# Optimization experiments

Hardware: AMD Instinct MI355X
Metric: run time of the kernel (lower is better)

## Reference

```python
import jax, jax.numpy as jnp
import numpy as np

NC = 80          # classes
REG_MAX = 16     # DFL bins
NK = 51          # 17*3 keypoint channels
KPT_SHAPE = (17, 3)
MAX_DET = 100
CONF_THRES = 0.25
STRIDES = (8, 16, 32)


def _conv1x1(f, w, b):
    # f: (B,C,H,W), w: (O,C), b: (O,) -> (B,O,H,W)
    return jnp.einsum('bchw,oc->bohw', f, w) + b[None, :, None, None]


def _make_anchors(shapes, strides, offset=0.5):
    pts, sts = [], []
    for (h, w), s in zip(shapes, strides):
        sx = jnp.arange(w, dtype=jnp.float32) + offset
        sy = jnp.arange(h, dtype=jnp.float32) + offset
        gy, gx = jnp.meshgrid(sy, sx, indexing='ij')
        pts.append(jnp.stack([gx, gy], -1).reshape(-1, 2))
        sts.append(jnp.full((h * w, 1), float(s), jnp.float32))
    # transposed as in _new_inference: anchors (2,A), strides (1,A)
    return jnp.concatenate(pts, 0).T, jnp.concatenate(sts, 0).T


def setup_inputs() -> dict:
    key = jax.random.key(0)
    ks = jax.random.split(key, 16)
    ch = (128, 256, 512)
    hw = ((80, 80), (40, 40), (20, 20))
    d = {}
    for i, (c, (h, w)) in enumerate(zip(ch, hw)):
        d[f'x{i}'] = jax.random.normal(ks[i], (16, c, h, w), jnp.float32)
    k = 3
    for name, oc in (('cv2', 4 * REG_MAX), ('cv3', NC), ('cv4', NK)):
        for i, c in enumerate(ch):
            d[f'{name}_w{i}'] = jax.random.normal(ks[k], (oc, c), jnp.float32) * 0.02
            d[f'{name}_b{i}'] = jnp.zeros((oc,), jnp.float32)
            k += 1
    return d


def reference(x0, x1, x2,
              cv2_w0, cv2_b0, cv2_w1, cv2_b1, cv2_w2, cv2_b2,
              cv3_w0, cv3_b0, cv3_w1, cv3_b1, cv3_w2, cv3_b2,
              cv4_w0, cv4_b0, cv4_w1, cv4_b1, cv4_w2, cv4_b2):
    feats = [x0, x1, x2]
    cv2 = [(cv2_w0, cv2_b0), (cv2_w1, cv2_b1), (cv2_w2, cv2_b2)]
    cv3 = [(cv3_w0, cv3_b0), (cv3_w1, cv3_b1), (cv3_w2, cv3_b2)]
    cv4 = [(cv4_w0, cv4_b0), (cv4_w1, cv4_b1), (cv4_w2, cv4_b2)]
    bs = x0.shape[0]

    # keypoint branch: cat over levels -> (bs, nk, A)
    kpt = jnp.concatenate(
        [_conv1x1(f, w, b).reshape(bs, NK, -1) for f, (w, b) in zip(feats, cv4)], -1)
    # box+cls branch -> (bs, 4*reg_max+nc, A)
    xcat = jnp.concatenate(
        [jnp.concatenate([_conv1x1(f, *cv2[i]), _conv1x1(f, *cv3[i])], 1).reshape(bs, 4 * REG_MAX + NC, -1)
         for i, f in enumerate(feats)], -1)
    box, cls = xcat[:, :4 * REG_MAX], xcat[:, 4 * REG_MAX:]

    shapes = [(f.shape[2], f.shape[3]) for f in feats]
    anchors, strides = _make_anchors(shapes, STRIDES)  # (2,A), (1,A)
    A = anchors.shape[1]

    # DFL decode: softmax over reg_max bins, expectation w/ arange weights
    p = jax.nn.softmax(box.reshape(bs, 4, REG_MAX, A), axis=2)
    dist = jnp.einsum('bfra,r->bfa', p, jnp.arange(REG_MAX, dtype=jnp.float32))
    lt, rb = dist[:, :2], dist[:, 2:]
    x1y1 = anchors[None] - lt
    x2y2 = anchors[None] + rb
    # xywh box coding, scaled by strides
    dbox = jnp.concatenate([(x1y1 + x2y2) * 0.5, x2y2 - x1y1], 1) * strides[None]  # (bs,4,A)

    # keypoint decode (Pose.kpts_decode, ndim==3)
    y = kpt.reshape(bs, KPT_SHAPE[0], KPT_SHAPE[1], A)
    kxy = (y[:, :, :2] * 2.0 + (anchors[None, None] - 0.5)) * strides[None, None]
    kv = jax.nn.sigmoid(y[:, :, 2:3])
    pred_kpts = jnp.concatenate([kxy, kv], 2).reshape(bs, NK, A).transpose(0, 2, 1)  # (bs,A,nk)

    # EfficientIdxNMS_TRT stand-in: sigmoid scores (score_activation=1),
    # class-agnostic deterministic top-k selection by best class score.
    scores = jax.nn.sigmoid(cls.transpose(0, 2, 1))  # (bs,A,nc)
    max_s = scores.max(-1)
    cls_id = jnp.argmax(scores, -1)
    top_s, top_i = jax.lax.top_k(max_s, MAX_DET)     # (bs,MAX_DET)
    num_dets = (top_s > CONF_THRES).sum(-1).astype(jnp.int32)[:, None]
    det_boxes = jnp.take_along_axis(dbox.transpose(0, 2, 1), top_i[..., None], 1)  # (bs,MAX_DET,4)
    det_classes = jnp.take_along_axis(cls_id, top_i, 1).astype(jnp.int32)
    # irregular keypoint gather via det indices (the pred_kpts[bs_indices, det_indices] step)
    det_kpts = jnp.take_along_axis(pred_kpts, top_i[..., None], 1).reshape(bs, MAX_DET, *KPT_SHAPE)
    return num_dets, det_boxes, top_s, det_classes, det_kpts
```

## Files before the change

kernel.cpp:

```cpp
#include <hip/hip_runtime.h>
#include <hip/hip_bf16.h>

#define NC 80
#define NK 51
#define REG_MAX 16
#define MAX_DET 100
#define A_TOT 8400
#define BS 16

#define OUT_NUM 0
#define OUT_BOX 16
#define OUT_SCORE (16 + 16*MAX_DET*4)
#define OUT_CLASS (OUT_SCORE + 16*MAX_DET)
#define OUT_KPT (OUT_CLASS + 16*MAX_DET)

static __device__ __forceinline__ unsigned long long mk_key(unsigned u, int a) {
    return ((unsigned long long)u << 32) | (unsigned)(0x7FFFFFFF - a);
}

__global__ __launch_bounds__(512) void scores_fused(
    const float* __restrict__ x0, const float* __restrict__ x1, const float* __restrict__ x2,
    const float* __restrict__ w0, const float* __restrict__ w1, const float* __restrict__ w2,
    const float* __restrict__ bias0, const float* __restrict__ bias1, const float* __restrict__ bias2,
    float* __restrict__ max_s,
    int* __restrict__ cls_id)
{
    __shared__ float rm[8][256];
    __shared__ int   ri[8][256];

    int bid = blockIdx.x;
    const float *x, *w, *bias; int C, A, a_off, b, tile;
    if (bid < 32) {
        x = x2; w = w2; bias = bias2; C = 512; A = 400; a_off = 8000;
        b = bid >> 1; tile = bid & 1;
    } else if (bid < 144) {
        int r = bid - 32;
        x = x1; w = w1; bias = bias1; C = 256; A = 1600; a_off = 6400;
        b = r / 7; tile = r - b * 7;
    } else {
        int r = bid - 144;
        x = x0; w = w0; bias = bias0; C = 128; A = 6400; a_off = 0;
        b = r / 25; tile = r - b * 25;
    }
    int a0 = tile * 256;

    int t = threadIdx.x;
    int lane = t & 63;
    int wv = t >> 6;
    int oc0 = wv * 10;

    int aa = a0 + lane * 4; if (aa > A - 4) aa = A - 4;
    const float* xb = x + (long)b * C * A + aa;

    int wrow = oc0 + (lane >> 5);
    int wcol = lane & 31;

    float acc[10][4];
#pragma unroll
    for (int j = 0; j < 10; ++j) {
        float bv = bias[oc0 + j];
        acc[j][0] = bv; acc[j][1] = bv; acc[j][2] = bv; acc[j][3] = bv;
    }

    int nchunk = C >> 5;
    float wcur[5], wnxt[5];
#pragma unroll
    for (int r2 = 0; r2 < 5; ++r2)
        wcur[r2] = w[(wrow + 2 * r2) * C + wcol];

    for (int kc = 0; kc < nchunk; ++kc) {
        int cbase = kc * 32;
        if (kc + 1 < nchunk) {
#pragma unroll
            for (int r2 = 0; r2 < 5; ++r2)
                wnxt[r2] = w[(wrow + 2 * r2) * C + cbase + 32 + wcol];
        }

#pragma unroll 2
        for (int c4 = 0; c4 < 32; c4 += 4) {
            const float* fp = xb + (long)(cbase + c4) * A;
            float4 f0 = *(const float4*)(fp);
            float4 f1 = *(const float4*)(fp + A);
            float4 f2 = *(const float4*)(fp + 2 * A);
            float4 f3 = *(const float4*)(fp + 3 * A);
#pragma unroll
            for (int j = 0; j < 10; ++j) {
                int rr = j >> 1;
                int hi = (j & 1) << 5;
                float ws0 = __int_as_float(__builtin_amdgcn_readlane(__float_as_int(wcur[rr]), hi + c4 + 0));
                float ws1 = __int_as_float(__builtin_amdgcn_readlane(__float_as_int(wcur[rr]), hi + c4 + 1));
                float ws2 = __int_as_float(__builtin_amdgcn_readlane(__float_as_int(wcur[rr]), hi + c4 + 2));
                float ws3 = __int_as_float(__builtin_amdgcn_readlane(__float_as_int(wcur[rr]), hi + c4 + 3));
                acc[j][0] = fmaf(ws0, f0.x, acc[j][0]);
                acc[j][0] = fmaf(ws1, f1.x, acc[j][0]);
                acc[j][0] = fmaf(ws2, f2.x, acc[j][0]);
                acc[j][0] = fmaf(ws3, f3.x, acc[j][0]);
                acc[j][1] = fmaf(ws0, f0.y, acc[j][1]);
                acc[j][1] = fmaf(ws1, f1.y, acc[j][1]);
                acc[j][1] = fmaf(ws2, f2.y, acc[j][1]);
                acc[j][1] = fmaf(ws3, f3.y, acc[j][1]);
                acc[j][2] = fmaf(ws0, f0.z, acc[j][2]);
                acc[j][2] = fmaf(ws1, f1.z, acc[j][2]);
                acc[j][2] = fmaf(ws2, f2.z, acc[j][2]);
                acc[j][2] = fmaf(ws3, f3.z, acc[j][2]);
                acc[j][3] = fmaf(ws0, f0.w, acc[j][3]);
                acc[j][3] = fmaf(ws1, f1.w, acc[j][3]);
                acc[j][3] = fmaf(ws2, f2.w, acc[j][3]);
                acc[j][3] = fmaf(ws3, f3.w, acc[j][3]);
            }
        }

        if (kc + 1 < nchunk) {
#pragma unroll
            for (int r2 = 0; r2 < 5; ++r2) wcur[r2] = wnxt[r2];
        }
    }

#pragma unroll
    for (int q = 0; q < 4; ++q) {
        float m = acc[0][q]; int mi = 0;
#pragma unroll
        for (int j = 1; j < 10; ++j)
            if (acc[j][q] > m) { m = acc[j][q]; mi = j; }
        rm[wv][lane * 4 + q] = m;
        ri[wv][lane * 4 + q] = oc0 + mi;
    }
    __syncthreads();

    if (t < 256) {
        float bm = rm[0][t]; int bi = ri[0][t];
#pragma unroll
        for (int v = 1; v < 8; ++v) {
            float om = rm[v][t];
            if (om > bm) { bm = om; bi = ri[v][t]; }
        }
        int ga = a0 + t;
        if (ga < A) {
            max_s[b * A_TOT + a_off + ga] = 1.0f / (1.0f + expf(-bm));
            cls_id[b * A_TOT + a_off + ga] = bi;
        }
    }
}

__global__ __launch_bounds__(1024) void topk_kernel(
    const float* __restrict__ max_s,
    const int* __restrict__ cls_id,
    float* __restrict__ out,
    int* __restrict__ top_idx)
{
    int b = blockIdx.x;
    int t = threadIdx.x;
    int wv = t >> 6;

    __shared__ unsigned hist[16 * 256];
    __shared__ unsigned suffix[256];
    __shared__ int tieIdx[A_TOT];
    __shared__ unsigned long long highKeys[128];
    __shared__ unsigned long long finalKeys[128];
    __shared__ int wmin[16];
    __shared__ unsigned s_prefix;
    __shared__ int s_k, s_selD, s_nHigh, s_nTie, s_cnt, s_bcast;

    unsigned u[9];
    bool val[9];
#pragma unroll
    for (int i = 0; i < 9; ++i) {
        int a = t + i * 1024;
        val[i] = (a < A_TOT);
        u[i] = val[i] ? __float_as_uint(max_s[b * A_TOT + a]) : 0u;
    }

    if (t == 0) { s_prefix = 0; s_k = MAX_DET; s_nHigh = 0; s_nTie = 0; s_cnt = 0; }

    for (int pass = 0; pass < 4; ++pass) {
#pragma unroll
        for (int j = 0; j < 4; ++j) hist[t + j * 1024] = 0;
        if (t == 0) s_selD = 0;
        __syncthreads();

        unsigned pre = s_prefix;
        int k = s_k;
        int shHi = 32 - 8 * pass;
        int shD = 24 - 8 * pass;
#pragma unroll
        for (int i = 0; i < 9; ++i) {
            if (val[i]) {
                bool cand = (pass == 0) ? true : ((u[i] >> shHi) == pre);
                if (cand)
                    atomicAdd(&hist[(wv << 8) + ((u[i] >> shD) & 0xFF)], 1u);
            }
        }
        __syncthreads();

        if (t < 256) {
            unsigned s = 0;
#pragma unroll
            for (int w = 0; w < 16; ++w) s += hist[(w << 8) + t];
            suffix[t] = s;
        }
        __syncthreads();
        for (int off = 1; off < 256; off <<= 1) {
            unsigned v = 0;
            if (t < 256) v = suffix[t] + ((t + off < 256) ? suffix[t + off] : 0u);
            __syncthreads();
            if (t < 256) suffix[t] = v;
            __syncthreads();
        }
        if (t < 256 && suffix[t] >= (unsigned)k) atomicMax(&s_selD, t);
        __syncthreads();
        if (t == 0) {
            int d = s_selD;
            s_k = k - ((d < 255) ? (int)suffix[d + 1] : 0);
            s_prefix = (pre << 8) | (unsigned)d;
        }
        __syncthreads();
    }

    unsigned cut = s_prefix;
    int r = s_k;

#pragma unroll
    for (int i = 0; i < 9; ++i) {
        if (val[i]) {
            int a = t + i * 1024;
            if (u[i] > cut) {
                int p = atomicAdd(&s_nHigh, 1);
                highKeys[p] = mk_key(u[i], a);
            } else if (u[i] == cut) {
                int p = atomicAdd(&s_nTie, 1);
                tieIdx[p] = a;
            }
        }
    }
    __syncthreads();
    int m = s_nHigh;
    int nt = s_nTie;

    if (t < 128) finalKeys[t] = 0ull;
    __syncthreads();
    if (t < m) finalKeys[t] = highKeys[t];

    if (nt == r) {
        if (t < nt) finalKeys[m + t] = mk_key(cut, tieIdx[t]);
        __syncthreads();
    } else {
        __syncthreads();
        for (int j = 0; j < r; ++j) {
            int mn = 0x7FFFFFFF;
            for (int p = t; p < nt; p += 1024) mn = min(mn, tieIdx[p]);
            for (int off = 32; off > 0; off >>= 1) mn = min(mn, __shfl_down(mn, off, 64));
            if ((t & 63) == 0) wmin[wv] = mn;
            __syncthreads();
            if (t == 0) {
                int v = wmin[0];
#pragma unroll
                for (int w = 1; w < 16; ++w) v = min(v, wmin[w]);
                s_bcast = v;
                finalKeys[m + j] = mk_key(cut, v);
            }
            __syncthreads();
            int v = s_bcast;
            for (int p = t; p < nt; p += 1024)
                if (tieIdx[p] == v) tieIdx[p] = 0x7FFFFFFF;
            __syncthreads();
        }
    }

    for (int ksz = 2; ksz <= 128; ksz <<= 1) {
        for (int j = ksz >> 1; j > 0; j >>= 1) {
            if (t < 128) {
                int ixj = t ^ j;
                if (ixj > t) {
                    bool desc = ((t & ksz) == 0);
                    unsigned long long x = finalKeys[t], y = finalKeys[ixj];
                    bool sw = desc ? (x < y) : (x > y);
                    if (sw) { finalKeys[t] = y; finalKeys[ixj] = x; }
                }
            }
            __syncthreads();
        }
    }

    if (t < MAX_DET) {
        unsigned long long kk = finalKeys[t];
        float sc = __uint_as_float((unsigned)(kk >> 32));
        int a = 0x7FFFFFFF - (int)(kk & 0xFFFFFFFFull);
        out[OUT_SCORE + b * MAX_DET + t] = sc;
        out[OUT_CLASS + b * MAX_DET + t] = (float)cls_id[b * A_TOT + a];
        top_idx[b * MAX_DET + t] = a;
        if (sc > 0.25f) atomicAdd(&s_cnt, 1);
    }
    __syncthreads();
    if (t == 0) out[OUT_NUM + b] = (float)s_cnt;
}

__global__ __launch_bounds__(128) void decode_kernel(
    const float* __restrict__ x0, const float* __restrict__ x1, const float* __restrict__ x2,
    const float* __restrict__ w2_0, const float* __restrict__ b2_0,
    const float* __restrict__ w2_1, const float* __restrict__ b2_1,
    const float* __restrict__ w2_2, const float* __restrict__ b2_2,
    const float* __restrict__ w4_0, const float* __restrict__ b4_0,
    const float* __restrict__ w4_1, const float* __restrict__ b4_1,
    const float* __restrict__ w4_2, const float* __restrict__ b4_2,
    const int* __restrict__ top_idx,
    float* __restrict__ out)
{
    int b = blockIdx.y;
    int k = blockIdx.x;
    int a = top_idx[b * MAX_DET + k];

    const float* x; const float* w2; const float* bb2; const float* w4; const float* bb4;
    int C, A, W, a_local; float stride;
    if (a < 6400)      { x = x0; C = 128; A = 6400; W = 80; stride = 8.0f;  a_local = a;        w2 = w2_0; bb2 = b2_0; w4 = w4_0; bb4 = b4_0; }
    else if (a < 8000) { x = x1; C = 256; A = 1600; W = 40; stride = 16.0f; a_local = a - 6400; w2 = w2_1; bb2 = b2_1; w4 = w4_1; bb4 = b4_1; }
    else               { x = x2; C = 512; A = 400;  W = 20; stride = 32.0f; a_local = a - 8000; w2 = w2_2; bb2 = b2_2; w4 = w4_2; bb4 = b4_2; }

    __shared__ float fs[512];
    __shared__ float logits[64];
    __shared__ float kraw[NK];
    __shared__ float dist[4];

    int t = threadIdx.x;
    for (int c = t; c < C; c += 128)
        fs[c] = x[((long)b * C + c) * A + a_local];
    __syncthreads();

    if (t < 64 + NK) {
        const float* wrow; float acc;
        if (t < 64) { wrow = w2 + t * C; acc = bb2[t]; }
        else        { wrow = w4 + (t - 64) * C; acc = bb4[t - 64]; }
        for (int c = 0; c < C; ++c) acc = fmaf(wrow[c], fs[c], acc);
        if (t < 64) logits[t] = acc;
        else        kraw[t - 64] = acc;
    }
    __syncthreads();

    if (t < 4) {
        float mx = logits[t * 16];
#pragma unroll
        for (int r = 1; r < 16; ++r) mx = fmaxf(mx, logits[t * 16 + r]);
        float se = 0.0f, sw = 0.0f;
#pragma unroll
        for (int r = 0; r < 16; ++r) {
            float e = expf(logits[t * 16 + r] - mx);
            se += e; sw += e * (float)r;
        }
        dist[t] = sw / se;
    }
    __syncthreads();

    float ax = (float)(a_local % W) + 0.5f;
    float ay = (float)(a_local / W) + 0.5f;

    if (t == 0) {
        float x1c = ax - dist[0], y1c = ay - dist[1];
        float x2c = ax + dist[2], y2c = ay + dist[3];
        float* ob = out + OUT_BOX + ((long)b * MAX_DET + k) * 4;
        ob[0] = (x1c + x2c) * 0.5f * stride;
        ob[1] = (y1c + y2c) * 0.5f * stride;
        ob[2] = (x2c - x1c) * stride;
        ob[3] = (y2c - y1c) * stride;
    }
    if (t < 17) {
        float vx = kraw[t * 3], vy = kraw[t * 3 + 1], vv = kraw[t * 3 + 2];
        float gx = ax - 0.5f, gy = ay - 0.5f;
        float* ok = out + OUT_KPT + (((long)b * MAX_DET + k) * 17 + t) * 3;
        ok[0] = (vx * 2.0f + gx) * stride;
        ok[1] = (vy * 2.0f + gy) * stride;
        ok[2] = 1.0f / (1.0f + expf(-vv));
    }
}

extern "C" void kernel_launch(void* const* d_in, const int* in_sizes, int n_in,
                              void* d_out, int out_size, void* d_ws, size_t ws_size,
                              hipStream_t stream) {
    const float* x0 = (const float*)d_in[0];
    const float* x1 = (const float*)d_in[1];
    const float* x2 = (const float*)d_in[2];
    const float* w2[3] = {(const float*)d_in[3], (const float*)d_in[5], (const float*)d_in[7]};
    const float* b2[3] = {(const float*)d_in[4], (const float*)d_in[6], (const float*)d_in[8]};
    const float* w3[3] = {(const float*)d_in[9], (const float*)d_in[11], (const float*)d_in[13]};
    const float* b3[3] = {(const float*)d_in[10], (const float*)d_in[12], (const float*)d_in[14]};
    const float* w4[3] = {(const float*)d_in[15], (const float*)d_in[17], (const float*)d_in[19]};
    const float* b4[3] = {(const float*)d_in[16], (const float*)d_in[18], (const float*)d_in[20]};

    float* out = (float*)d_out;

    float* ws_maxs = (float*)d_ws;
    int* ws_cls = (int*)(ws_maxs + BS * A_TOT);
    int* ws_top = (int*)(ws_cls + BS * A_TOT);

    scores_fused<<<dim3(544), 512, 0, stream>>>(
        x0, x1, x2, w3[0], w3[1], w3[2], b3[0], b3[1], b3[2], ws_maxs, ws_cls);
    topk_kernel<<<dim3(BS), 1024, 0, stream>>>(ws_maxs, ws_cls, out, ws_top);
    decode_kernel<<<dim3(MAX_DET, BS), 128, 0, stream>>>(
        x0, x1, x2,
        w2[0], b2[0], w2[1], b2[1], w2[2], b2[2],
        w4[0], b4[0], w4[1], b4[1], w4[2], b4[2],
        ws_top, out);
}
```

Before: 312.5 us.

## Retile class-score conv into smaller templated blocks with scalar weight loads

Rewrites the fused class-score 1x1 conv kernel as a templated per-level tile function with compile-time C and A. Blocks shrink from 512 to 256 threads and the grid grows to 1120 blocks. Each wave now computes 20 output channels for 1 or 2 anchors per lane, instead of 10 channels for 4 anchors. Weights are loaded with wave-uniform (scalar) addresses instead of being broadcast via readlane, and per-level constants are specialized at compile time. The aim is more parallelism and occupancy across the CUs, at the cost of narrower feature loads and more weight-load traffic per FMA.

```diff
diff --git a/kernel.cpp b/kernel.cpp
--- a/kernel.cpp
+++ b/kernel.cpp
@@ -18,127 +18,107 @@
     return ((unsigned long long)u << 32) | (unsigned)(0x7FFFFFFF - a);
 }
 
-__global__ __launch_bounds__(512) void scores_fused(
+template<int C, int A, int PP>
+static __device__ __forceinline__ void score_tile(
+    const float* __restrict__ x, const float* __restrict__ w,
+    const float* __restrict__ bias,
+    int b, int a0, int a_off,
+    float* __restrict__ max_s, int* __restrict__ cls_id,
+    float (*rm)[128], int (*ri)[128])
+{
+    int t = threadIdx.x;
+    int lane = t & 63;
+    int wv = t >> 6;
+    int oc0 = __builtin_amdgcn_readfirstlane(wv * 20);
+
+    int aa = a0 + lane * PP;
+    if (aa > A - PP) aa = A - PP;
+    const float* xb = x + (long)b * C * A + aa;
+    const float* wb = w + oc0 * C;
+
+    float acc[20][PP];
+#pragma unroll
+    for (int j = 0; j < 20; ++j) {
+        float bv = bias[oc0 + j];
+#pragma unroll
+        for (int q = 0; q < PP; ++q) acc[j][q] = bv;
+    }
+
+#pragma unroll 2
+    for (int c = 0; c < C; c += 4) {
+        float f[4][PP];
+#pragma unroll
+        for (int cc = 0; cc < 4; ++cc) {
+            const float* fp = xb + (long)(c + cc) * A;
+            if (PP == 2) {
+                float2 v = *(const float2*)fp;
+                f[cc][0] = v.x; f[cc][1] = v.y;
+            } else {
+                f[cc][0] = *fp;
+            }
+        }
+#pragma unroll
+        for (int j = 0; j < 20; ++j) {
+            const float* wr = wb + j * C + c;
+            float w0 = wr[0], w1 = wr[1], w2 = wr[2], w3 = wr[3];
+#pragma unroll
+            for (int q = 0; q < PP; ++q) {
+                acc[j][q] = fmaf(w0, f[0][q], acc[j][q]);
+                acc[j][q] = fmaf(w1, f[1][q], acc[j][q]);
+                acc[j][q] = fmaf(w2, f[2][q], acc[j][q]);
+                acc[j][q] = fmaf(w3, f[3][q], acc[j][q]);
+            }
+        }
+    }
+
+#pragma unroll
+    for (int q = 0; q < PP; ++q) {
+        float m = acc[0][q]; int mi = 0;
+#pragma unroll
+        for (int j = 1; j < 20; ++j)
+            if (acc[j][q] > m) { m = acc[j][q]; mi = j; }
+        rm[wv][lane * PP + q] = m;
+        ri[wv][lane * PP + q] = oc0 + mi;
+    }
+    __syncthreads();
+
+    if (t < 64 * PP) {
+        float bm = rm[0][t]; int bi = ri[0][t];
+#pragma unroll
+        for (int v = 1; v < 4; ++v) {
+            float om = rm[v][t];
+            if (om > bm) { bm = om; bi = ri[v][t]; }
+        }
+        int ga = a0 + t;
+        if (ga < A) {
+            max_s[b * A_TOT + a_off + ga] = 1.0f / (1.0f + expf(-bm));
+            cls_id[b * A_TOT + a_off + ga] = bi;
+        }
+    }
+}
+
+__global__ __launch_bounds__(256, 4) void scores_fused(
     const float* __restrict__ x0, const float* __restrict__ x1, const float* __restrict__ x2,
     const float* __restrict__ w0, const float* __restrict__ w1, const float* __restrict__ w2,
     const float* __restrict__ bias0, const float* __restrict__ bias1, const float* __restrict__ bias2,
     float* __restrict__ max_s,
     int* __restrict__ cls_id)
 {
-    __shared__ float rm[8][256];
-    __shared__ int   ri[8][256];
+    __shared__ float rm[4][128];
+    __shared__ int   ri[4][128];
 
     int bid = blockIdx.x;
-    const float *x, *w, *bias; int C, A, a_off, b, tile;
-    if (bid < 32) {
-        x = x2; w = w2; bias = bias2; C = 512; A = 400; a_off = 8000;
-        b = bid >> 1; tile = bid & 1;
-    } else if (bid < 144) {
-        int r = bid - 32;
-        x = x1; w = w1; bias = bias1; C = 256; A = 1600; a_off = 6400;
-        b = r / 7; tile = r - b * 7;
+    if (bid < 112) {
+        int b = bid / 7, tile = bid - b * 7;
+        score_tile<512, 400, 1>(x2, w2, bias2, b, tile * 64, 8000, max_s, cls_id, rm, ri);
+    } else if (bid < 320) {
+        int r = bid - 112;
+        int b = r / 13, tile = r - b * 13;
+        score_tile<256, 1600, 2>(x1, w1, bias1, b, tile * 128, 6400, max_s, cls_id, rm, ri);
     } else {
-        int r = bid - 144;
-        x = x0; w = w0; bias = bias0; C = 128; A = 6400; a_off = 0;
-        b = r / 25; tile = r - b * 25;
-    }
-    int a0 = tile * 256;
-
-    int t = threadIdx.x;
-    int lane = t & 63;
-    int wv = t >> 6;
-    int oc0 = wv * 10;
-
-    int aa = a0 + lane * 4; if (aa > A - 4) aa = A - 4;
-    const float* xb = x + (long)b * C * A + aa;
-
-    int wrow = oc0 + (lane >> 5);
-    int wcol = lane & 31;
-
-    float acc[10][4];
-#pragma unroll
-    for (int j = 0; j < 10; ++j) {
-        float bv = bias[oc0 + j];
-        acc[j][0] = bv; acc[j][1] = bv; acc[j][2] = bv; acc[j][3] = bv;
-    }
-
-    int nchunk = C >> 5;
-    float wcur[5], wnxt[5];
-#pragma unroll
-    for (int r2 = 0; r2 < 5; ++r2)
-        wcur[r2] = w[(wrow + 2 * r2) * C + wcol];
-
-    for (int kc = 0; kc < nchunk; ++kc) {
-        int cbase = kc * 32;
-        if (kc + 1 < nchunk) {
-#pragma unroll
-            for (int r2 = 0; r2 < 5; ++r2)
-                wnxt[r2] = w[(wrow + 2 * r2) * C + cbase + 32 + wcol];
-        }
-
-#pragma unroll 2
-        for (int c4 = 0; c4 < 32; c4 += 4) {
-            const float* fp = xb + (long)(cbase + c4) * A;
-            float4 f0 = *(const float4*)(fp);
-            float4 f1 = *(const float4*)(fp + A);
-            float4 f2 = *(const float4*)(fp + 2 * A);
-            float4 f3 = *(const float4*)(fp + 3 * A);
-#pragma unroll
-            for (int j = 0; j < 10; ++j) {
-                int rr = j >> 1;
-                int hi = (j & 1) << 5;
-                float ws0 = __int_as_float(__builtin_amdgcn_readlane(__float_as_int(wcur[rr]), hi + c4 + 0));
-                float ws1 = __int_as_float(__builtin_amdgcn_readlane(__float_as_int(wcur[rr]), hi + c4 + 1));
-                float ws2 = __int_as_float(__builtin_amdgcn_readlane(__float_as_int(wcur[rr]), hi + c4 + 2));
-                float ws3 = __int_as_float(__builtin_amdgcn_readlane(__float_as_int(wcur[rr]), hi + c4 + 3));
-                acc[j][0] = fmaf(ws0, f0.x, acc[j][0]);
-                acc[j][0] = fmaf(ws1, f1.x, acc[j][0]);
-                acc[j][0] = fmaf(ws2, f2.x, acc[j][0]);
-                acc[j][0] = fmaf(ws3, f3.x, acc[j][0]);
-                acc[j][1] = fmaf(ws0, f0.y, acc[j][1]);
-                acc[j][1] = fmaf(ws1, f1.y, acc[j][1]);
-                acc[j][1] = fmaf(ws2, f2.y, acc[j][1]);
-                acc[j][1] = fmaf(ws3, f3.y, acc[j][1]);
-                acc[j][2] = fmaf(ws0, f0.z, acc[j][2]);
-                acc[j][2] = fmaf(ws1, f1.z, acc[j][2]);
-                acc[j][2] = fmaf(ws2, f2.z, acc[j][2]);
-                acc[j][2] = fmaf(ws3, f3.z, acc[j][2]);
-                acc[j][3] = fmaf(ws0, f0.w, acc[j][3]);
-                acc[j][3] = fmaf(ws1, f1.w, acc[j][3]);
-                acc[j][3] = fmaf(ws2, f2.w, acc[j][3]);
-                acc[j][3] = fmaf(ws3, f3.w, acc[j][3]);
-            }
-        }
-
-        if (kc + 1 < nchunk) {
-#pragma unroll
-            for (int r2 = 0; r2 < 5; ++r2) wcur[r2] = wnxt[r2];
-        }
-    }
-
-#pragma unroll
-    for (int q = 0; q < 4; ++q) {
-        float m = acc[0][q]; int mi = 0;
-#pragma unroll
-        for (int j = 1; j < 10; ++j)
-            if (acc[j][q] > m) { m = acc[j][q]; mi = j; }
-        rm[wv][lane * 4 + q] = m;
-        ri[wv][lane * 4 + q] = oc0 + mi;
-    }
-    __syncthreads();
-
-    if (t < 256) {
-        float bm = rm[0][t]; int bi = ri[0][t];
-#pragma unroll
-        for (int v = 1; v < 8; ++v) {
-            float om = rm[v][t];
-            if (om > bm) { bm = om; bi = ri[v][t]; }
-        }
-        int ga = a0 + t;
-        if (ga < A) {
-            max_s[b * A_TOT + a_off + ga] = 1.0f / (1.0f + expf(-bm));
-            cls_id[b * A_TOT + a_off + ga] = bi;
-        }
+        int r = bid - 320;
+        int b = r / 50, tile = r - b * 50;
+        score_tile<128, 6400, 2>(x0, w0, bias0, b, tile * 128, 0, max_s, cls_id, rm, ri);
     }
 }
 
@@ -390,7 +370,7 @@
     int* ws_cls = (int*)(ws_maxs + BS * A_TOT);
     int* ws_top = (int*)(ws_cls + BS * A_TOT);
 
-    scores_fused<<<dim3(544), 512, 0, stream>>>(
+    scores_fused<<<dim3(1120), 256, 0, stream>>>(
         x0, x1, x2, w3[0], w3[1], w3[2], b3[0], b3[1], b3[2], ws_maxs, ws_cls);
     topk_kernel<<<dim3(BS), 1024, 0, stream>>>(ws_maxs, ws_cls, out, ws_top);
     decode_kernel<<<dim3(MAX_DET, BS), 128, 0, stream>>>(
```

After: 389.8 us. 24.7% more time.

## Stage conv weights in shared memory and template score kernel on C and A

Applied to the files above, without the earlier changes.

Weight rows for each 32-channel chunk are now loaded cooperatively into LDS and read as float4, replacing the per-lane register prefetch plus readlane broadcasts. The scoring body becomes a template over channel count and anchor count, so the compiler sees constant strides and trip counts. Launch bounds now request 3 blocks per CU. This trades the scalar readlane traffic for two block barriers per chunk and extra LDS reads, and drops the overlap of the next chunk's weight loads with compute.

```diff
diff --git a/kernel.cpp b/kernel.cpp
--- a/kernel.cpp
+++ b/kernel.cpp
@@ -18,42 +18,22 @@
     return ((unsigned long long)u << 32) | (unsigned)(0x7FFFFFFF - a);
 }
 
-__global__ __launch_bounds__(512) void scores_fused(
-    const float* __restrict__ x0, const float* __restrict__ x1, const float* __restrict__ x2,
-    const float* __restrict__ w0, const float* __restrict__ w1, const float* __restrict__ w2,
-    const float* __restrict__ bias0, const float* __restrict__ bias1, const float* __restrict__ bias2,
-    float* __restrict__ max_s,
-    int* __restrict__ cls_id)
+template<int C, int A>
+static __device__ __forceinline__ void score_tile(
+    const float* __restrict__ x, const float* __restrict__ w,
+    const float* __restrict__ bias,
+    int b, int a0, int a_off,
+    float* __restrict__ max_s, int* __restrict__ cls_id,
+    float* __restrict__ wsh, float (*rm)[256], int (*ri)[256])
 {
-    __shared__ float rm[8][256];
-    __shared__ int   ri[8][256];
-
-    int bid = blockIdx.x;
-    const float *x, *w, *bias; int C, A, a_off, b, tile;
-    if (bid < 32) {
-        x = x2; w = w2; bias = bias2; C = 512; A = 400; a_off = 8000;
-        b = bid >> 1; tile = bid & 1;
-    } else if (bid < 144) {
-        int r = bid - 32;
-        x = x1; w = w1; bias = bias1; C = 256; A = 1600; a_off = 6400;
-        b = r / 7; tile = r - b * 7;
-    } else {
-        int r = bid - 144;
-        x = x0; w = w0; bias = bias0; C = 128; A = 6400; a_off = 0;
-        b = r / 25; tile = r - b * 25;
-    }
-    int a0 = tile * 256;
-
     int t = threadIdx.x;
     int lane = t & 63;
     int wv = t >> 6;
     int oc0 = wv * 10;
 
-    int aa = a0 + lane * 4; if (aa > A - 4) aa = A - 4;
+    int aa = a0 + lane * 4;
+    if (aa > A - 4) aa = A - 4;
     const float* xb = x + (long)b * C * A + aa;
-
-    int wrow = oc0 + (lane >> 5);
-    int wcol = lane & 31;
 
     float acc[10][4];
 #pragma unroll
@@ -63,18 +43,20 @@
     }
 
     int nchunk = C >> 5;
-    float wcur[5], wnxt[5];
-#pragma unroll
-    for (int r2 = 0; r2 < 5; ++r2)
-        wcur[r2] = w[(wrow + 2 * r2) * C + wcol];
-
     for (int kc = 0; kc < nchunk; ++kc) {
         int cbase = kc * 32;
-        if (kc + 1 < nchunk) {
-#pragma unroll
-            for (int r2 = 0; r2 < 5; ++r2)
-                wnxt[r2] = w[(wrow + 2 * r2) * C + cbase + 32 + wcol];
-        }
+        if (kc) __syncthreads();
+#pragma unroll
+        for (int i = 0; i < 2; ++i) {
+            int idx = t + i * 512;
+            if (idx < 640) {
+                int oc = idx >> 3;
+                int q = idx & 7;
+                float4 v = *(const float4*)(w + oc * C + cbase + q * 4);
+                *(float4*)(&wsh[idx * 4]) = v;
+            }
+        }
+        __syncthreads();
 
 #pragma unroll 2
         for (int c4 = 0; c4 < 32; c4 += 4) {
@@ -85,34 +67,24 @@
             float4 f3 = *(const float4*)(fp + 3 * A);
 #pragma unroll
             for (int j = 0; j < 10; ++j) {
-                int rr = j >> 1;
-                int hi = (j & 1) << 5;
-                float ws0 = __int_as_float(__builtin_amdgcn_readlane(__float_as_int(wcur[rr]), hi + c4 + 0));
-                float ws1 = __int_as_float(__builtin_amdgcn_readlane(__float_as_int(wcur[rr]), hi + c4 + 1));
-                float ws2 = __int_as_float(__builtin_amdgcn_readlane(__float_as_int(wcur[rr]), hi + c4 + 2));
-                float ws3 = __int_as_float(__builtin_amdgcn_readlane(__float_as_int(wcur[rr]), hi + c4 + 3));
-                acc[j][0] = fmaf(ws0, f0.x, acc[j][0]);
-                acc[j][0] = fmaf(ws1, f1.x, acc[j][0]);
-                acc[j][0] = fmaf(ws2, f2.x, acc[j][0]);
-                acc[j][0] = fmaf(ws3, f3.x, acc[j][0]);
-                acc[j][1] = fmaf(ws0, f0.y, acc[j][1]);
-                acc[j][1] = fmaf(ws1, f1.y, acc[j][1]);
-                acc[j][1] = fmaf(ws2, f2.y, acc[j][1]);
-                acc[j][1] = fmaf(ws3, f3.y, acc[j][1]);
-                acc[j][2] = fmaf(ws0, f0.z, acc[j][2]);
-                acc[j][2] = fmaf(ws1, f1.z, acc[j][2]);
-                acc[j][2] = fmaf(ws2, f2.z, acc[j][2]);
-                acc[j][2] = fmaf(ws3, f3.z, acc[j][2]);
-                acc[j][3] = fmaf(ws0, f0.w, acc[j][3]);
-                acc[j][3] = fmaf(ws1, f1.w, acc[j][3]);
-                acc[j][3] = fmaf(ws2, f2.w, acc[j][3]);
-                acc[j][3] = fmaf(ws3, f3.w, acc[j][3]);
-            }
-        }
-
-        if (kc + 1 < nchunk) {
-#pragma unroll
-            for (int r2 = 0; r2 < 5; ++r2) wcur[r2] = wnxt[r2];
+                float4 w4 = *(const float4*)(&wsh[(oc0 + j) * 32 + c4]);
+                acc[j][0] = fmaf(w4.x, f0.x, acc[j][0]);
+                acc[j][0] = fmaf(w4.y, f1.x, acc[j][0]);
+                acc[j][0] = fmaf(w4.z, f2.x, acc[j][0]);
+                acc[j][0] = fmaf(w4.w, f3.x, acc[j][0]);
+                acc[j][1] = fmaf(w4.x, f0.y, acc[j][1]);
+                acc[j][1] = fmaf(w4.y, f1.y, acc[j][1]);
+                acc[j][1] = fmaf(w4.z, f2.y, acc[j][1]);
+                acc[j][1] = fmaf(w4.w, f3.y, acc[j][1]);
+                acc[j][2] = fmaf(w4.x, f0.z, acc[j][2]);
+                acc[j][2] = fmaf(w4.y, f1.z, acc[j][2]);
+                acc[j][2] = fmaf(w4.z, f2.z, acc[j][2]);
+                acc[j][2] = fmaf(w4.w, f3.z, acc[j][2]);
+                acc[j][3] = fmaf(w4.x, f0.w, acc[j][3]);
+                acc[j][3] = fmaf(w4.y, f1.w, acc[j][3]);
+                acc[j][3] = fmaf(w4.z, f2.w, acc[j][3]);
+                acc[j][3] = fmaf(w4.w, f3.w, acc[j][3]);
+            }
         }
     }
 
@@ -139,6 +111,32 @@
             max_s[b * A_TOT + a_off + ga] = 1.0f / (1.0f + expf(-bm));
             cls_id[b * A_TOT + a_off + ga] = bi;
         }
+    }
+}
+
+__global__ __launch_bounds__(512, 3) void scores_fused(
+    const float* __restrict__ x0, const float* __restrict__ x1, const float* __restrict__ x2,
+    const float* __restrict__ w0, const float* __restrict__ w1, const float* __restrict__ w2,
+    const float* __restrict__ bias0, const float* __restrict__ bias1, const float* __restrict__ bias2,
+    float* __restrict__ max_s,
+    int* __restrict__ cls_id)
+{
+    __shared__ float wsh[80 * 32];
+    __shared__ float rm[8][256];
+    __shared__ int   ri[8][256];
+
+    int bid = blockIdx.x;
+    if (bid < 32) {
+        int b = bid >> 1, tile = bid & 1;
+        score_tile<512, 400>(x2, w2, bias2, b, tile * 256, 8000, max_s, cls_id, wsh, rm, ri);
+    } else if (bid < 144) {
+        int r = bid - 32;
+        int b = r / 7, tile = r - b * 7;
+        score_tile<256, 1600>(x1, w1, bias1, b, tile * 256, 6400, max_s, cls_id, wsh, rm, ri);
+    } else {
+        int r = bid - 144;
+        int b = r / 25, tile = r - b * 25;
+        score_tile<128, 6400>(x0, w0, bias0, b, tile * 256, 0, max_s, cls_id, wsh, rm, ri);
     }
 }
 
```

Measured after the change: 305.8 us. 2.2% less time.
